# Kernel optimization log

Measured on AMD Instinct MI355X. Metric: run time of the kernel, lower is better.

Reference implementation:

```python
import jax, jax.numpy as jnp
import numpy as np

N_POINTS = 2_097_152  # ~1448x1448 sample points
N_CELLS = 5
N_SHAPES = 3 * N_CELLS * N_CELLS  # 75 primitives (tri, circle, ellipse per cell)


def _build_params():
    # Replicates the structure of VectorGraphicsRGB2IntegrandSlang.__init__:
    # per cell: triangle (11 floats), circle (8 floats), ellipse (9 floats).
    rng = np.random.default_rng(42)
    n, jf = N_CELLS, 1.0
    cw = 1.0 / n
    params = []
    for i in range(n):
        for j in range(n):
            bx = (i + 0.5) / n + (rng.random() - 0.5) * jf * cw
            by = (j + 0.5) / n + (rng.random() - 0.5) * jf * cw
            rad = 0.4 / n
            ang = np.sort(rng.random(3) * 2.0 * 3.14159)
            pxs = np.clip(bx + rad * np.cos(ang), 0.0, 1.0)
            pys = np.clip(by + rad * np.sin(ang), 0.0, 1.0)
            params += [1.0, pxs[0], pys[0], pxs[1], pys[1], pxs[2], pys[2], 0.0] + list(rng.random(3))
            cxx = (i + 0.5) / n + (rng.random() - 0.5) * jf * cw
            cyy = (j + 0.5) / n + (rng.random() - 0.5) * jf * cw
            cr = rng.random() * 0.1 / n + 0.05 / n
            cxx = min(max(cxx, cr), 1.0 - cr)
            cyy = min(max(cyy, cr), 1.0 - cr)
            params += [3.0, cxx, cyy, cr, 0.0] + list(rng.random(3))
            exx = (i + 0.5) / n + (rng.random() - 0.5) * jf * cw
            eyy = (j + 0.5) / n + (rng.random() - 0.5) * jf * cw
            erx = rng.random() * 0.12 / n + 0.04 / n
            ery = rng.random() * 0.12 / n + 0.04 / n
            exx = min(max(exx, erx), 1.0 - erx)
            eyy = min(max(eyy, ery), 1.0 - ery)
            params += [2.0, exx, eyy, erx, ery, 0.0] + list(rng.random(3))
    return np.asarray(params, dtype=np.float32)  # [700]


def setup_inputs() -> dict:
    key = jax.random.key(0)
    k1, _ = jax.random.split(key)
    x = jax.random.uniform(k1, (N_POINTS, 2), dtype=jnp.float32)  # points in [0,1]^2
    p = jnp.asarray(_build_params())
    return {"x": x, "p": p}


def reference(x, p):
    # Parse the fixed-layout parameter vector: 25 cells x 28 floats.
    cells = p.reshape(N_CELLS * N_CELLS, 28)
    tri, circ, ell = cells[:, :11], cells[:, 11:19], cells[:, 19:]
    px, py = x[:, 0:1], x[:, 1:2]  # [N,1] broadcast against [25] shapes

    # Triangle containment: consistent sign of the three edge cross products.
    ax, ay, bx, by, cx, cy = (tri[:, k] for k in range(1, 7))
    e0 = (px - ax) * (by - ay) - (py - ay) * (bx - ax)  # [N,25]
    e1 = (px - bx) * (cy - by) - (py - by) * (cx - bx)
    e2 = (px - cx) * (ay - cy) - (py - cy) * (ax - cx)
    tri_in = ((e0 >= 0) & (e1 >= 0) & (e2 >= 0)) | ((e0 <= 0) & (e1 <= 0) & (e2 <= 0))

    # Circle containment.
    ocx, ocy, orr = circ[:, 1], circ[:, 2], circ[:, 3]
    circ_in = (px - ocx) ** 2 + (py - ocy) ** 2 <= orr ** 2

    # Ellipse containment.
    ecx, ecy, erx, ery = ell[:, 1], ell[:, 2], ell[:, 3], ell[:, 4]
    ell_in = ((px - ecx) / erx) ** 2 + ((py - ecy) / ery) ** 2 <= 1.0

    # Interleave per-cell in shader evaluation order: triangle, circle, ellipse.
    inside = jnp.stack([tri_in, circ_in, ell_in], axis=2).reshape(x.shape[0], N_SHAPES)
    colors = jnp.stack([tri[:, 8:11], circ[:, 5:8], ell[:, 6:9]], axis=1).reshape(N_SHAPES, 3)

    last = (N_SHAPES - 1) - jnp.argmax(inside[:, ::-1], axis=1)  # [N]
    any_in = inside.any(axis=1)
    return jnp.where(any_in[:, None], colors[last], jnp.zeros((), x.dtype))  # [N,3]
```

## Files before the change

### kernel.cpp

```cpp
#include <hip/hip_runtime.h>

#pragma clang fp contract(off)

#define NPTS 2097152
#define PPT  4
#define NTHREADS (NPTS / PPT)

#define P_PACK 0
#define P_COL  980
#define P_ETRI 1284
#define P_ECIR 1584
#define P_EELL 1684

#define LDS_FLOATS 1284

#define EPS_T 1e-6f
#define EPS_C 1e-7f
#define EPS_E 1e-5f

__global__ void vg_precompute(const float* __restrict__ p, float* __restrict__ ws) {
    int t = threadIdx.x;
    if (t < 49) {
        int gi = t / 7, gj = t % 7;
        float* o = ws + P_PACK + t * 20;
        if (gi >= 1 && gi <= 5 && gj >= 1 && gj <= 5) {
            int c = (gi - 1) * 5 + (gj - 1);
            const float* cell = p + c * 28;
            float ax = cell[1], ay = cell[2], bx = cell[3], by = cell[4], cx = cell[5], cy = cell[6];
            float d0y = by - ay, d0x = bx - ax;
            float d1y = cy - by, d1x = cx - bx;
            float d2y = ay - cy, d2x = ax - cx;
            o[0] = d0y; o[1] = -d0x; o[2] = (float)((double)ay * (double)d0x - (double)ax * (double)d0y);
            o[3] = d1y; o[4] = -d1x; o[5] = (float)((double)by * (double)d1x - (double)bx * (double)d1y);
            o[6] = d2y; o[7] = -d2x; o[8] = (float)((double)cy * (double)d2x - (double)cx * (double)d2y);
            o[9]  = cell[12]; o[10] = cell[13]; o[11] = cell[14] * cell[14];
            o[12] = cell[20]; o[13] = cell[21]; o[14] = 1.0f / cell[22]; o[15] = 1.0f / cell[23];
        } else {
            o[0] = 0.f; o[1] = 0.f; o[2] = 10.f;
            o[3] = 0.f; o[4] = 0.f; o[5] = -10.f;
            o[6] = 0.f; o[7] = 0.f; o[8] = 0.f;
            o[9] = 0.f; o[10] = 0.f; o[11] = -10.f;
            o[12] = 1000.f; o[13] = 1000.f; o[14] = 1.f; o[15] = 1.f;
        }
        o[16] = 0.f; o[17] = 0.f; o[18] = 0.f; o[19] = 0.f;
    } else if (t < 74) {
        int c = t - 49;
        const float* cell = p + c * 28;
        float ax = cell[1], ay = cell[2], bx = cell[3], by = cell[4], cx = cell[5], cy = cell[6];
        float* o = ws + P_ETRI + c * 12;
        o[0] = ax; o[1] = ay; o[2]  = by - ay; o[3]  = bx - ax;
        o[4] = bx; o[5] = by; o[6]  = cy - by; o[7]  = cx - bx;
        o[8] = cx; o[9] = cy; o[10] = ay - cy; o[11] = ax - cx;
        float* col = ws + P_COL + (3 * c + 0) * 4;
        col[0] = cell[8]; col[1] = cell[9]; col[2] = cell[10]; col[3] = 0.f;
    } else if (t < 99) {
        int c = t - 74;
        const float* cell = p + c * 28;
        float orr = cell[14];
        float* o = ws + P_ECIR + c * 4;
        o[0] = cell[12]; o[1] = cell[13]; o[2] = orr * orr; o[3] = 0.f;
        float* col = ws + P_COL + (3 * c + 1) * 4;
        col[0] = cell[16]; col[1] = cell[17]; col[2] = cell[18]; col[3] = 0.f;
    } else if (t < 124) {
        int c = t - 99;
        const float* cell = p + c * 28;
        float* o = ws + P_EELL + c * 8;
        o[0] = cell[20]; o[1] = cell[21]; o[2] = 0.f; o[3] = 0.f;
        o[4] = cell[22]; o[5] = cell[23]; o[6] = 0.f; o[7] = 0.f;
        float* col = ws + P_COL + (3 * c + 2) * 4;
        col[0] = cell[25]; col[1] = cell[26]; col[2] = cell[27]; col[3] = 0.f;
    } else if (t == 124) {
        float* col = ws + P_COL + 75 * 4;
        col[0] = 0.f; col[1] = 0.f; col[2] = 0.f; col[3] = 0.f;
    }
}

__device__ __noinline__ int exact_point(float px, float py, int ihi, int jhi,
                                        const float* __restrict__ ws) {
    int idx = -1;
#pragma clang loop unroll(disable)
    for (int s = 0; s < 4; ++s) {
        int gi = ihi + (s >> 1), gj = jhi + (s & 1);
        if (gi < 1 || gi > 5 || gj < 1 || gj > 5) continue;
        int c = 5 * (gi - 1) + (gj - 1);
        const float* tc = ws + P_ETRI + c * 12;
        float e0 = (px - tc[0]) * tc[2]  - (py - tc[1]) * tc[3];
        float e1 = (px - tc[4]) * tc[6]  - (py - tc[5]) * tc[7];
        float e2 = (px - tc[8]) * tc[10] - (py - tc[9]) * tc[11];
        bool tin = (e0 >= 0.f && e1 >= 0.f && e2 >= 0.f) ||
                   (e0 <= 0.f && e1 <= 0.f && e2 <= 0.f);
        if (tin) idx = 3 * c;
        const float* cc = ws + P_ECIR + c * 4;
        float dx = px - cc[0], dy = py - cc[1];
        if (dx * dx + dy * dy <= cc[2]) idx = 3 * c + 1;
        const float* ec = ws + P_EELL + c * 8;
        float u = (px - ec[0]) / ec[4];
        float v = (py - ec[1]) / ec[5];
        if (u * u + v * v <= 1.0f) idx = 3 * c + 2;
    }
    return idx;
}

__global__ __launch_bounds__(256) void vg_main(const float* __restrict__ x,
                                               const float* __restrict__ ws,
                                               float* __restrict__ out) {
    __shared__ float lds[LDS_FLOATS];
    int tl = threadIdx.x;
    int t  = blockIdx.x * 256 + tl;

    {
        float4* l4 = (float4*)lds;
        const float4* g4 = (const float4*)ws;
        l4[tl] = g4[tl];
        if (tl < LDS_FLOATS / 4 - 256) l4[256 + tl] = g4[256 + tl];
    }
    __syncthreads();

    const float4* x4 = (const float4*)x;
    float4 xa = x4[2 * t], xb = x4[2 * t + 1];
    float PX[PPT] = {xa.x, xa.z, xb.x, xb.z};
    float PY[PPT] = {xa.y, xa.w, xb.y, xb.w};
    int idx[PPT], ihi[PPT], jhi[PPT];
    bool unc[PPT];

#pragma unroll
    for (int k = 0; k < PPT; ++k) {
        idx[k] = -1; unc[k] = false;
        ihi[k] = (int)floorf(__builtin_fmaf(PX[k], 5.0f, 0.4025f));
        jhi[k] = (int)floorf(__builtin_fmaf(PY[k], 5.0f, 0.4025f));
    }

#pragma unroll
    for (int a = 0; a < 2; ++a) {
#pragma unroll
        for (int b = 0; b < 2; ++b) {
#pragma unroll
            for (int k = 0; k < PPT; ++k) {
                int gi = ihi[k] + a, gj = jhi[k] + b;
                const float4* c4 = (const float4*)(lds + (gi * 7 + gj) * 20);
                float4 q0 = c4[0], q1 = c4[1], q2 = c4[2], q3 = c4[3];
                float X = PX[k], Y = PY[k];

                float e0 = __builtin_fmaf(X, q0.x, __builtin_fmaf(Y, q0.y, q0.z));
                float e1 = __builtin_fmaf(X, q0.w, __builtin_fmaf(Y, q1.x, q1.y));
                float e2 = __builtin_fmaf(X, q1.z, __builtin_fmaf(Y, q1.w, q2.x));
                float lo = __builtin_fminf(__builtin_fminf(e0, e1), e2);
                float hi = __builtin_fmaxf(__builtin_fmaxf(e0, e1), e2);
                bool ts = (lo >= EPS_T) || (hi <= -EPS_T);
                bool tr = (lo >= -EPS_T) || (hi <= EPS_T);
                unc[k] = unc[k] || (ts != tr);
                int sid = 15 * gi + 3 * gj - 18;
                idx[k] = ts ? sid : idx[k];

                float dx = X - q2.y, dy = Y - q2.z;
                float tcirc = __builtin_fmaf(dx, dx, dy * dy);
                unc[k] = unc[k] || (__builtin_fabsf(tcirc - q2.w) < EPS_C);
                idx[k] = (tcirc <= q2.w) ? sid + 1 : idx[k];

                float ex = X - q3.x, ey = Y - q3.y;
                float u = ex * q3.z, v = ey * q3.w;
                float te = __builtin_fmaf(u, u, v * v);
                unc[k] = unc[k] || (__builtin_fabsf(te - 1.0f) < EPS_E);
                idx[k] = (te <= 1.0f) ? sid + 2 : idx[k];
            }
        }
    }

#pragma unroll
    for (int k = 0; k < PPT; ++k)
        if (__builtin_expect(unc[k], 0))
            idx[k] = exact_point(PX[k], PY[k], ihi[k], jhi[k], ws);

    const float4* col4 = (const float4*)(lds + P_COL);
    float4 c0 = col4[idx[0] < 0 ? 75 : idx[0]];
    float4 c1 = col4[idx[1] < 0 ? 75 : idx[1]];
    float4 c2 = col4[idx[2] < 0 ? 75 : idx[2]];
    float4 c3 = col4[idx[3] < 0 ? 75 : idx[3]];

    float4* out4 = (float4*)out;
    out4[3 * t + 0] = make_float4(c0.x, c0.y, c0.z, c1.x);
    out4[3 * t + 1] = make_float4(c1.y, c1.z, c2.x, c2.y);
    out4[3 * t + 2] = make_float4(c2.z, c3.x, c3.y, c3.z);
}

extern "C" void kernel_launch(void* const* d_in, const int* in_sizes, int n_in,
                              void* d_out, int out_size, void* d_ws, size_t ws_size,
                              hipStream_t stream) {
    const float* x = (const float*)d_in[0];
    const float* p = (const float*)d_in[1];
    float* out = (float*)d_out;
    float* ws  = (float*)d_ws;

    vg_precompute<<<1, 128, 0, stream>>>(p, ws);
    vg_main<<<NTHREADS / 256, 256, 0, stream>>>(x, ws, out);
}
```

Baseline: 86.17 us.

## Fuse parameter precompute into main kernel and process eight points per thread

Removes the separate single-block precompute launch: each block now builds the packed shape table and color table directly into LDS from the raw parameter vector, and the rare exact fallback reads raw parameters. Points per thread rise from four to eight, halving the grid and amortizing the per-block setup. The cost is redundant per-block precompute (including double-precision math), a longer serial prologue before the sync, and higher register pressure that may lower occupancy.

New measurement: 91.62 us. 6.3% more time.

```diff
diff --git a/kernel.cpp b/kernel.cpp
--- a/kernel.cpp
+++ b/kernel.cpp
@@ -3,26 +3,51 @@
 #pragma clang fp contract(off)
 
 #define NPTS 2097152
-#define PPT  4
+#define PPT  8
 #define NTHREADS (NPTS / PPT)
 
-#define P_PACK 0
-#define P_COL  980
-#define P_ETRI 1284
-#define P_ECIR 1584
-#define P_EELL 1684
-
-#define LDS_FLOATS 1284
+#define L_COL  980
+#define LDS_FLOATS (980 + 304)
 
 #define EPS_T 1e-6f
 #define EPS_C 1e-7f
 #define EPS_E 1e-5f
 
-__global__ void vg_precompute(const float* __restrict__ p, float* __restrict__ ws) {
-    int t = threadIdx.x;
-    if (t < 49) {
-        int gi = t / 7, gj = t % 7;
-        float* o = ws + P_PACK + t * 20;
+__device__ __noinline__ int exact_point(float px, float py, int ihi, int jhi,
+                                        const float* __restrict__ p) {
+    int idx = -1;
+#pragma clang loop unroll(disable)
+    for (int s = 0; s < 4; ++s) {
+        int gi = ihi + (s >> 1), gj = jhi + (s & 1);
+        if (gi < 1 || gi > 5 || gj < 1 || gj > 5) continue;
+        int c = 5 * (gi - 1) + (gj - 1);
+        const float* cell = p + 28 * c;
+        float ax = cell[1], ay = cell[2], bx = cell[3], by = cell[4], cx = cell[5], cy = cell[6];
+        float e0 = (px - ax) * (by - ay) - (py - ay) * (bx - ax);
+        float e1 = (px - bx) * (cy - by) - (py - by) * (cx - bx);
+        float e2 = (px - cx) * (ay - cy) - (py - cy) * (ax - cx);
+        bool tin = (e0 >= 0.f && e1 >= 0.f && e2 >= 0.f) ||
+                   (e0 <= 0.f && e1 <= 0.f && e2 <= 0.f);
+        if (tin) idx = 3 * c;
+        float dx = px - cell[12], dy = py - cell[13];
+        if (dx * dx + dy * dy <= cell[14] * cell[14]) idx = 3 * c + 1;
+        float u = (px - cell[20]) / cell[22];
+        float v = (py - cell[21]) / cell[23];
+        if (u * u + v * v <= 1.0f) idx = 3 * c + 2;
+    }
+    return idx;
+}
+
+__global__ __launch_bounds__(256) void vg_fused(const float* __restrict__ x,
+                                                const float* __restrict__ p,
+                                                float* __restrict__ out) {
+    __shared__ float lds[LDS_FLOATS];
+    int tl = threadIdx.x;
+    int t  = blockIdx.x * 256 + tl;
+
+    if (tl < 49) {
+        int gi = tl / 7, gj = tl % 7;
+        float* o = lds + tl * 20;
         if (gi >= 1 && gi <= 5 && gj >= 1 && gj <= 5) {
             int c = (gi - 1) * 5 + (gj - 1);
             const float* cell = p + c * 28;
@@ -43,86 +68,31 @@
             o[12] = 1000.f; o[13] = 1000.f; o[14] = 1.f; o[15] = 1.f;
         }
         o[16] = 0.f; o[17] = 0.f; o[18] = 0.f; o[19] = 0.f;
-    } else if (t < 74) {
-        int c = t - 49;
-        const float* cell = p + c * 28;
-        float ax = cell[1], ay = cell[2], bx = cell[3], by = cell[4], cx = cell[5], cy = cell[6];
-        float* o = ws + P_ETRI + c * 12;
-        o[0] = ax; o[1] = ay; o[2]  = by - ay; o[3]  = bx - ax;
-        o[4] = bx; o[5] = by; o[6]  = cy - by; o[7]  = cx - bx;
-        o[8] = cx; o[9] = cy; o[10] = ay - cy; o[11] = ax - cx;
-        float* col = ws + P_COL + (3 * c + 0) * 4;
-        col[0] = cell[8]; col[1] = cell[9]; col[2] = cell[10]; col[3] = 0.f;
-    } else if (t < 99) {
-        int c = t - 74;
-        const float* cell = p + c * 28;
-        float orr = cell[14];
-        float* o = ws + P_ECIR + c * 4;
-        o[0] = cell[12]; o[1] = cell[13]; o[2] = orr * orr; o[3] = 0.f;
-        float* col = ws + P_COL + (3 * c + 1) * 4;
-        col[0] = cell[16]; col[1] = cell[17]; col[2] = cell[18]; col[3] = 0.f;
-    } else if (t < 124) {
-        int c = t - 99;
-        const float* cell = p + c * 28;
-        float* o = ws + P_EELL + c * 8;
-        o[0] = cell[20]; o[1] = cell[21]; o[2] = 0.f; o[3] = 0.f;
-        o[4] = cell[22]; o[5] = cell[23]; o[6] = 0.f; o[7] = 0.f;
-        float* col = ws + P_COL + (3 * c + 2) * 4;
-        col[0] = cell[25]; col[1] = cell[26]; col[2] = cell[27]; col[3] = 0.f;
-    } else if (t == 124) {
-        float* col = ws + P_COL + 75 * 4;
-        col[0] = 0.f; col[1] = 0.f; col[2] = 0.f; col[3] = 0.f;
     }
-}
-
-__device__ __noinline__ int exact_point(float px, float py, int ihi, int jhi,
-                                        const float* __restrict__ ws) {
-    int idx = -1;
-#pragma clang loop unroll(disable)
-    for (int s = 0; s < 4; ++s) {
-        int gi = ihi + (s >> 1), gj = jhi + (s & 1);
-        if (gi < 1 || gi > 5 || gj < 1 || gj > 5) continue;
-        int c = 5 * (gi - 1) + (gj - 1);
-        const float* tc = ws + P_ETRI + c * 12;
-        float e0 = (px - tc[0]) * tc[2]  - (py - tc[1]) * tc[3];
-        float e1 = (px - tc[4]) * tc[6]  - (py - tc[5]) * tc[7];
-        float e2 = (px - tc[8]) * tc[10] - (py - tc[9]) * tc[11];
-        bool tin = (e0 >= 0.f && e1 >= 0.f && e2 >= 0.f) ||
-                   (e0 <= 0.f && e1 <= 0.f && e2 <= 0.f);
-        if (tin) idx = 3 * c;
-        const float* cc = ws + P_ECIR + c * 4;
-        float dx = px - cc[0], dy = py - cc[1];
-        if (dx * dx + dy * dy <= cc[2]) idx = 3 * c + 1;
-        const float* ec = ws + P_EELL + c * 8;
-        float u = (px - ec[0]) / ec[4];
-        float v = (py - ec[1]) / ec[5];
-        if (u * u + v * v <= 1.0f) idx = 3 * c + 2;
-    }
-    return idx;
-}
-
-__global__ __launch_bounds__(256) void vg_main(const float* __restrict__ x,
-                                               const float* __restrict__ ws,
-                                               float* __restrict__ out) {
-    __shared__ float lds[LDS_FLOATS];
-    int tl = threadIdx.x;
-    int t  = blockIdx.x * 256 + tl;
-
-    {
-        float4* l4 = (float4*)lds;
-        const float4* g4 = (const float4*)ws;
-        l4[tl] = g4[tl];
-        if (tl < LDS_FLOATS / 4 - 256) l4[256 + tl] = g4[256 + tl];
+    if (tl >= 128 && tl < 204) {
+        int e = tl - 128;
+        float* col = lds + L_COL + e * 4;
+        if (e < 75) {
+            int c = e / 3, kind = e - 3 * c;
+            const float* cell = p + c * 28;
+            int base = (kind == 0) ? 8 : (kind == 1) ? 16 : 25;
+            col[0] = cell[base]; col[1] = cell[base + 1]; col[2] = cell[base + 2];
+        } else {
+            col[0] = 0.f; col[1] = 0.f; col[2] = 0.f;
+        }
+        col[3] = 0.f;
     }
     __syncthreads();
 
     const float4* x4 = (const float4*)x;
-    float4 xa = x4[2 * t], xb = x4[2 * t + 1];
-    float PX[PPT] = {xa.x, xa.z, xb.x, xb.z};
-    float PY[PPT] = {xa.y, xa.w, xb.y, xb.w};
+    float PX[PPT], PY[PPT];
     int idx[PPT], ihi[PPT], jhi[PPT];
     bool unc[PPT];
-
+#pragma unroll
+    for (int k = 0; k < PPT; k += 2) {
+        float4 v = x4[4 * t + k / 2];
+        PX[k] = v.x; PY[k] = v.y; PX[k + 1] = v.z; PY[k + 1] = v.w;
+    }
 #pragma unroll
     for (int k = 0; k < PPT; ++k) {
         idx[k] = -1; unc[k] = false;
@@ -153,9 +123,9 @@
                 idx[k] = ts ? sid : idx[k];
 
                 float dx = X - q2.y, dy = Y - q2.z;
-                float tcirc = __builtin_fmaf(dx, dx, dy * dy);
-                unc[k] = unc[k] || (__builtin_fabsf(tcirc - q2.w) < EPS_C);
-                idx[k] = (tcirc <= q2.w) ? sid + 1 : idx[k];
+                float tc = __builtin_fmaf(dx, dx, dy * dy);
+                unc[k] = unc[k] || (__builtin_fabsf(tc - q2.w) < EPS_C);
+                idx[k] = (tc <= q2.w) ? sid + 1 : idx[k];
 
                 float ex = X - q3.x, ey = Y - q3.y;
                 float u = ex * q3.z, v = ey * q3.w;
@@ -169,18 +139,21 @@
 #pragma unroll
     for (int k = 0; k < PPT; ++k)
         if (__builtin_expect(unc[k], 0))
-            idx[k] = exact_point(PX[k], PY[k], ihi[k], jhi[k], ws);
+            idx[k] = exact_point(PX[k], PY[k], ihi[k], jhi[k], p);
 
-    const float4* col4 = (const float4*)(lds + P_COL);
-    float4 c0 = col4[idx[0] < 0 ? 75 : idx[0]];
-    float4 c1 = col4[idx[1] < 0 ? 75 : idx[1]];
-    float4 c2 = col4[idx[2] < 0 ? 75 : idx[2]];
-    float4 c3 = col4[idx[3] < 0 ? 75 : idx[3]];
+    const float4* col4 = (const float4*)(lds + L_COL);
+    float4 C[PPT];
+#pragma unroll
+    for (int k = 0; k < PPT; ++k) C[k] = col4[idx[k] < 0 ? 75 : idx[k]];
 
     float4* out4 = (float4*)out;
-    out4[3 * t + 0] = make_float4(c0.x, c0.y, c0.z, c1.x);
-    out4[3 * t + 1] = make_float4(c1.y, c1.z, c2.x, c2.y);
-    out4[3 * t + 2] = make_float4(c2.z, c3.x, c3.y, c3.z);
+#pragma unroll
+    for (int k = 0; k < PPT; k += 4) {
+        int o = 6 * t + 3 * (k / 4);
+        out4[o + 0] = make_float4(C[k].x, C[k].y, C[k].z, C[k + 1].x);
+        out4[o + 1] = make_float4(C[k + 1].y, C[k + 1].z, C[k + 2].x, C[k + 2].y);
+        out4[o + 2] = make_float4(C[k + 2].z, C[k + 3].x, C[k + 3].y, C[k + 3].z);
+    }
 }
 
 extern "C" void kernel_launch(void* const* d_in, const int* in_sizes, int n_in,
@@ -189,8 +162,7 @@
     const float* x = (const float*)d_in[0];
     const float* p = (const float*)d_in[1];
     float* out = (float*)d_out;
-    float* ws  = (float*)d_ws;
+    (void)d_ws; (void)ws_size;
 
-    vg_precompute<<<1, 128, 0, stream>>>(p, ws);
-    vg_main<<<NTHREADS / 256, 256, 0, stream>>>(x, ws, out);
+    vg_fused<<<NTHREADS / 256, 256, 0, stream>>>(x, p, out);
 }
```
